# Kernel tuning notes

Hardware: AMD Instinct MI355X
Metric: run time of the kernel (lower is better)

## Reference

```python
import jax, jax.numpy as jnp
import numpy as np

N_PDE = 4096
SENSOR_RANGE = 0.08
WINDOW = int(SENSOR_RANGE * N_PDE)   # 327
HALF = WINDOW // 2                   # 163
RESIZE_LEN = 20
FREQS = jnp.array([1.0, 2.0, 4.0, 8.0], dtype=jnp.float32)
EPS = 1e-6  # flax GroupNorm default epsilon
U_MAX, V_MAX = 40.0, 1.0
N_AGENTS = 262144


def setup_inputs() -> dict:
    key = jax.random.key(0)
    ks = jax.random.split(key, 16)

    def w(k, shape):
        fan_in = shape[0]
        return (jax.random.normal(k, shape, jnp.float32) / np.float32(np.sqrt(fan_in)))

    return {
        "z_curr": jax.random.normal(ks[0], (N_PDE,), jnp.float32),
        "z_target": jax.random.normal(ks[1], (N_PDE,), jnp.float32),
        "xi_curr": jax.random.uniform(ks[2], (N_AGENTS,), jnp.float32),
        # branch net (features=[256,256]), each layer: Dense + GroupNorm(1 group) + tanh
        "bW0": w(ks[3], (2 * RESIZE_LEN, 256)), "bb0": jnp.zeros((256,), jnp.float32),
        "bs0": jnp.ones((256,), jnp.float32), "bB0": jnp.zeros((256,), jnp.float32),
        "bW1": w(ks[4], (256, 256)), "bb1": jnp.zeros((256,), jnp.float32),
        "bs1": jnp.ones((256,), jnp.float32), "bB1": jnp.zeros((256,), jnp.float32),
        # trunk net: 8 -> 32 -> 32
        "tW0": w(ks[5], (8, 32)), "tb0": jnp.zeros((32,), jnp.float32),
        "tW1": w(ks[6], (32, 32)), "tb1": jnp.zeros((32,), jnp.float32),
        # combined head: (256+32) -> 32, then two 32 -> 1 heads
        "cW": w(ks[7], (256 + 32, 32)), "cb": jnp.zeros((32,), jnp.float32),
        "uW": w(ks[8], (32, 1)), "ub": jnp.zeros((1,), jnp.float32),
        "vW": w(ks[9], (32, 1)), "vb": jnp.zeros((1,), jnp.float32),
    }


def _local_obs(padded_error, xi):
    # per-agent dynamic slice + finite-difference gradient + bilinear resize
    center = (xi * (N_PDE - 1)).astype(jnp.int32) + HALF
    start = center - HALF
    p_err = jax.lax.dynamic_slice(padded_error, (start,), (WINDOW,))
    p_grad = jnp.gradient(p_err)
    p_err = jax.image.resize(p_err, (RESIZE_LEN,), method='bilinear')
    p_grad = jax.image.resize(p_grad, (RESIZE_LEN,), method='bilinear')
    return jnp.concatenate([p_err, p_grad])  # [40]


def _groupnorm1(x, scale, bias):
    # GroupNorm(num_groups=1) applied per-sample over the feature axis
    mu = jnp.mean(x, axis=-1, keepdims=True)
    var = jnp.var(x, axis=-1, keepdims=True)
    return (x - mu) * jax.lax.rsqrt(var + EPS) * scale + bias


def reference(z_curr, z_target, xi_curr,
              bW0, bb0, bs0, bB0, bW1, bb1, bs1, bB1,
              tW0, tb0, tW1, tb1, cW, cb, uW, ub, vW, vb):
    error = z_curr - z_target
    padded = jnp.pad(error, (HALF, HALF), mode='edge')  # [N_PDE + 2*HALF]

    patches = jax.vmap(lambda xi: _local_obs(padded, xi))(xi_curr)  # [A, 40]

    # branch net
    h = jnp.tanh(_groupnorm1(patches @ bW0 + bb0, bs0, bB0))  # [A, 256]
    h = jnp.tanh(_groupnorm1(h @ bW1 + bb1, bs1, bB1))        # [A, 256]

    # trunk net
    angle = xi_curr[:, None] * FREQS * jnp.pi                 # [A, 4]
    enc = jnp.concatenate([jnp.sin(angle), jnp.cos(angle)], axis=-1)  # [A, 8]
    enc = jnp.tanh(enc @ tW0 + tb0)
    enc = jnp.tanh(enc @ tW1 + tb1)                           # [A, 32]

    combined = jnp.concatenate([h, enc], axis=-1)             # [A, 288]
    x = jnp.tanh(combined @ cW + cb)                          # [A, 32]
    u_raw = (x @ uW + ub).squeeze(-1)
    v_raw = (x @ vW + vb).squeeze(-1)
    return (U_MAX * jnp.tanh(u_raw), V_MAX * jnp.tanh(v_raw))
```

## Files before the change

kernel.cpp:

```cpp
#include <hip/hip_runtime.h>

#define NP      4096
#define WINDOW  327
#define HALF    163
#define RL      20
#define NA      262144
#define GN_EPS  1e-6f
#define R       8
#define NBLK    (NP / R)
#define NT      512

__device__ __forceinline__ float tanh_fast(float x) {
  float e = __expf(2.0f * x);
  return 1.0f - 2.0f / (e + 1.0f);
}

__device__ __forceinline__ void wave_sum2(float& a, float& b) {
#pragma unroll
  for (int m = 1; m < 64; m <<= 1) {
    a += __shfl_xor(a, m, 64);
    b += __shfl_xor(b, m, 64);
  }
}

#define L_PART  0
#define L_ESP   0
#define L_OBS   336
#define L_HBUF  16384
#define L_HCL   18464
#define L_TOT   18752

__global__ __launch_bounds__(NT, 4) void dc_table(
    const float* __restrict__ zc,  const float* __restrict__ zt,
    const float* __restrict__ bW0, const float* __restrict__ bb0,
    const float* __restrict__ bs0, const float* __restrict__ bB0,
    const float* __restrict__ bW1, const float* __restrict__ bb1,
    const float* __restrict__ bs1, const float* __restrict__ bB1,
    const float* __restrict__ tW0, const float* __restrict__ tb0,
    const float* __restrict__ tW1, const float* __restrict__ tb1,
    const float* __restrict__ cW,  const float* __restrict__ cb,
    const float* __restrict__ uW,  const float* __restrict__ ub,
    const float* __restrict__ vW,  const float* __restrict__ vb,
    float* __restrict__ tbl)
{
  __shared__ __align__(16) float sm[L_TOT];
  float* espan = sm + L_ESP;
  float* obsT  = sm + L_OBS;
  float* part  = sm + L_PART;
  float* hbuf  = sm + L_HBUF;
  float* hcL   = sm + L_HCL;

  const int tid = threadIdx.x;
  const int w   = tid >> 6;
  const int l   = tid & 63;
  const int s0  = blockIdx.x * R;

  if (tid < WINDOW + R - 1) {
    int c = s0 - HALF + tid;
    c = c < 0 ? 0 : (c > NP - 1 ? NP - 1 : c);
    espan[tid] = zc[c] - zt[c];
  }
  __syncthreads();

  {
    const float INV  = (float)WINDOW / (float)RL;
    const float RINV = (float)RL / (float)WINDOW;
    const int sub = tid & 7;
    const int g8  = tid >> 3;
#pragma unroll
    for (int it = 0; it < 5; ++it) {
      int task = it * 64 + g8;
      int q = task % (2 * RL);
      int r = task / (2 * RL);
      int qq = (q < RL) ? q : q - RL;
      float xs = ((float)qq + 0.5f) * INV - 0.5f;
      int jlo = (int)ceilf(xs - INV);  if (jlo < 0) jlo = 0;
      int jhi = (int)floorf(xs + INV); if (jhi > WINDOW - 1) jhi = WINDOW - 1;
      const float* p = espan + r;
      float wsum = 0.0f, vsum = 0.0f;
      for (int j = jlo + sub; j <= jhi; j += 8) {
        float wq = 1.0f - fabsf(xs - (float)j) * RINV;
        float v;
        if (q < RL) {
          v = p[j];
        } else {
          v = (j == 0) ? (p[1] - p[0]) :
              (j == WINDOW - 1) ? (p[WINDOW - 1] - p[WINDOW - 2]) :
              0.5f * (p[j + 1] - p[j - 1]);
        }
        wsum += wq;
        vsum += wq * v;
      }
#pragma unroll
      for (int m = 1; m < 8; m <<= 1) {
        wsum += __shfl_xor(wsum, m, 64);
        vsum += __shfl_xor(vsum, m, 64);
      }
      if (sub == 0) obsT[q * 8 + r] = vsum / wsum;
    }
  }
  __syncthreads();

  float acc[R][4];

#pragma unroll
  for (int r = 0; r < R; ++r) { acc[r][0]=0.f; acc[r][1]=0.f; acc[r][2]=0.f; acc[r][3]=0.f; }
  for (int kk = 0; kk < 5; ++kk) {
    int k = w * 5 + kk;
    float4 wt = *(const float4*)&bW0[k * 256 + 4 * l];
    float4 o0 = *(const float4*)&obsT[k * 8];
    float4 o1 = *(const float4*)&obsT[k * 8 + 4];
    const float wv[4] = {wt.x, wt.y, wt.z, wt.w};
    const float ov[8] = {o0.x, o0.y, o0.z, o0.w, o1.x, o1.y, o1.z, o1.w};
#pragma unroll
    for (int r = 0; r < R; ++r)
#pragma unroll
      for (int j = 0; j < 4; ++j) acc[r][j] = fmaf(ov[r], wv[j], acc[r][j]);
  }
  __syncthreads();

#pragma unroll
  for (int r = 0; r < R; ++r)
    *(float4*)&part[(w << 11) + (r << 8) + 4 * l] = make_float4(acc[r][0], acc[r][1], acc[r][2], acc[r][3]);
  __syncthreads();
  {
    float4 b0 = *(const float4*)&bb0[4 * l];
    float val[4] = {b0.x, b0.y, b0.z, b0.w};
#pragma unroll
    for (int w2 = 0; w2 < 8; ++w2) {
      float4 p0 = *(const float4*)&part[(w2 << 11) + (w << 8) + 4 * l];
      val[0]+=p0.x; val[1]+=p0.y; val[2]+=p0.z; val[3]+=p0.w;
    }
    float s = 0.f, q = 0.f;
#pragma unroll
    for (int i = 0; i < 4; ++i) { s += val[i]; q += val[i] * val[i]; }
    wave_sum2(s, q);
    float mu  = s * (1.0f / 256.0f);
    float var = fmaxf(q * (1.0f / 256.0f) - mu * mu, 0.0f);
    float rv  = rsqrtf(var + GN_EPS);
    float4 sc0 = *(const float4*)&bs0[4 * l];
    float4 sh0 = *(const float4*)&bB0[4 * l];
    const float sc[4] = {sc0.x,sc0.y,sc0.z,sc0.w};
    const float sh[4] = {sh0.x,sh0.y,sh0.z,sh0.w};
    float h[4];
#pragma unroll
    for (int i = 0; i < 4; ++i) h[i] = tanh_fast((val[i] - mu) * rv * sc[i] + sh[i]);
    *(float4*)&hbuf[w * 260 + 4 * l] = make_float4(h[0], h[1], h[2], h[3]);
  }
  __syncthreads();

#pragma unroll
  for (int r = 0; r < R; ++r) { acc[r][0]=0.f; acc[r][1]=0.f; acc[r][2]=0.f; acc[r][3]=0.f; }
  for (int kk = 0; kk < 32; kk += 4) {
    int k0 = w * 32 + kk;
    float4 wt0 = *(const float4*)&bW1[(k0    ) * 256 + 4 * l];
    float4 wt1 = *(const float4*)&bW1[(k0 + 1) * 256 + 4 * l];
    float4 wt2 = *(const float4*)&bW1[(k0 + 2) * 256 + 4 * l];
    float4 wt3 = *(const float4*)&bW1[(k0 + 3) * 256 + 4 * l];
    float4 hr[R];
#pragma unroll
    for (int r = 0; r < R; ++r) hr[r] = *(const float4*)&hbuf[r * 260 + k0];
#pragma unroll
    for (int r = 0; r < R; ++r) {
      const float* hp = (const float*)&hr[r];
      acc[r][0] = fmaf(hp[0], wt0.x, acc[r][0]); acc[r][1] = fmaf(hp[0], wt0.y, acc[r][1]);
      acc[r][2] = fmaf(hp[0], wt0.z, acc[r][2]); acc[r][3] = fmaf(hp[0], wt0.w, acc[r][3]);
      acc[r][0] = fmaf(hp[1], wt1.x, acc[r][0]); acc[r][1] = fmaf(hp[1], wt1.y, acc[r][1]);
      acc[r][2] = fmaf(hp[1], wt1.z, acc[r][2]); acc[r][3] = fmaf(hp[1], wt1.w, acc[r][3]);
      acc[r][0] = fmaf(hp[2], wt2.x, acc[r][0]); acc[r][1] = fmaf(hp[2], wt2.y, acc[r][1]);
      acc[r][2] = fmaf(hp[2], wt2.z, acc[r][2]); acc[r][3] = fmaf(hp[2], wt2.w, acc[r][3]);
      acc[r][0] = fmaf(hp[3], wt3.x, acc[r][0]); acc[r][1] = fmaf(hp[3], wt3.y, acc[r][1]);
      acc[r][2] = fmaf(hp[3], wt3.z, acc[r][2]); acc[r][3] = fmaf(hp[3], wt3.w, acc[r][3]);
    }
  }

#pragma unroll
  for (int r = 0; r < R; ++r)
    *(float4*)&part[(w << 11) + (r << 8) + 4 * l] = make_float4(acc[r][0], acc[r][1], acc[r][2], acc[r][3]);
  __syncthreads();
  {
    float4 b0 = *(const float4*)&bb1[4 * l];
    float val[4] = {b0.x, b0.y, b0.z, b0.w};
#pragma unroll
    for (int w2 = 0; w2 < 8; ++w2) {
      float4 p0 = *(const float4*)&part[(w2 << 11) + (w << 8) + 4 * l];
      val[0]+=p0.x; val[1]+=p0.y; val[2]+=p0.z; val[3]+=p0.w;
    }
    float s = 0.f, q = 0.f;
#pragma unroll
    for (int i = 0; i < 4; ++i) { s += val[i]; q += val[i] * val[i]; }
    wave_sum2(s, q);
    float mu  = s * (1.0f / 256.0f);
    float var = fmaxf(q * (1.0f / 256.0f) - mu * mu, 0.0f);
    float rv  = rsqrtf(var + GN_EPS);
    float4 sc0 = *(const float4*)&bs1[4 * l];
    float4 sh0 = *(const float4*)&bB1[4 * l];
    const float sc[4] = {sc0.x,sc0.y,sc0.z,sc0.w};
    const float sh[4] = {sh0.x,sh0.y,sh0.z,sh0.w};
    float h[4];
#pragma unroll
    for (int i = 0; i < 4; ++i) h[i] = tanh_fast((val[i] - mu) * rv * sc[i] + sh[i]);
    *(float4*)&hbuf[w * 260 + 4 * l] = make_float4(h[0], h[1], h[2], h[3]);
  }
  __syncthreads();

  {
    int r  = w;
    int kg = l >> 3;
    int c  = (l & 7) * 4;
    float ga0 = 0.f, ga1 = 0.f, ga2 = 0.f, ga3 = 0.f;
#pragma unroll
    for (int ii = 0; ii < 8; ++ii) {
      int j  = (ii + kg) & 7;
      int kb = kg * 32 + 4 * j;
      float4 hv = *(const float4*)&hbuf[r * 260 + kb];
      const float hvv[4] = {hv.x, hv.y, hv.z, hv.w};
#pragma unroll
      for (int i2 = 0; i2 < 4; ++i2) {
        float4 cw = *(const float4*)&cW[(kb + i2) * 32 + c];
        ga0 = fmaf(hvv[i2], cw.x, ga0);
        ga1 = fmaf(hvv[i2], cw.y, ga1);
        ga2 = fmaf(hvv[i2], cw.z, ga2);
        ga3 = fmaf(hvv[i2], cw.w, ga3);
      }
    }
#pragma unroll
    for (int m = 8; m < 64; m <<= 1) {
      ga0 += __shfl_xor(ga0, m, 64);
      ga1 += __shfl_xor(ga1, m, 64);
      ga2 += __shfl_xor(ga2, m, 64);
      ga3 += __shfl_xor(ga3, m, 64);
    }
    if (l < 8) {
      float4 cbv = *(const float4*)&cb[c];
      *(float4*)&hcL[r * 36 + c] = make_float4(ga0 + cbv.x, ga1 + cbv.y, ga2 + cbv.z, ga3 + cbv.w);
    }
  }
  __syncthreads();

  if (tid < 128) {
    int v = tid >> 3, sub = tid & 7;
    int r = v >> 1, e = v & 1;
    int jg = s0 + r + e;
    float xe = (float)jg * (1.0f / 4095.0f);
    float enc[8];
#pragma unroll
    for (int k = 0; k < 4; ++k) {
      float fr = (float)(1 << k);
      float a = (xe * fr) * 3.14159265358979f;
      enc[k]     = sinf(a);
      enc[k + 4] = cosf(a);
    }
    int base = (tid & 63) & ~7;

    float t0v[4];
#pragma unroll
    for (int i = 0; i < 4; ++i) {
      int f = 4 * sub + i;
      float a = tb0[f];
#pragma unroll
      for (int k = 0; k < 8; ++k) a = fmaf(enc[k], tW0[k * 32 + f], a);
      t0v[i] = tanh_fast(a);
    }

    float t1v[4];
#pragma unroll
    for (int i = 0; i < 4; ++i) t1v[i] = tb1[4 * sub + i];
#pragma unroll
    for (int j8 = 0; j8 < 8; ++j8) {
#pragma unroll
      for (int i2 = 0; i2 < 4; ++i2) {
        float tv = __shfl(t0v[i2], base + j8, 64);
        int k = 4 * j8 + i2;
#pragma unroll
        for (int i = 0; i < 4; ++i) t1v[i] = fmaf(tv, tW1[k * 32 + 4 * sub + i], t1v[i]);
      }
    }
#pragma unroll
    for (int i = 0; i < 4; ++i) t1v[i] = tanh_fast(t1v[i]);

    float xvv[4];
#pragma unroll
    for (int i = 0; i < 4; ++i) xvv[i] = hcL[r * 36 + 4 * sub + i];
#pragma unroll
    for (int j8 = 0; j8 < 8; ++j8) {
#pragma unroll
      for (int i2 = 0; i2 < 4; ++i2) {
        float tv = __shfl(t1v[i2], base + j8, 64);
        int k = 4 * j8 + i2;
#pragma unroll
        for (int i = 0; i < 4; ++i) xvv[i] = fmaf(tv, cW[(256 + k) * 32 + 4 * sub + i], xvv[i]);
      }
    }
#pragma unroll
    for (int i = 0; i < 4; ++i) xvv[i] = tanh_fast(xvv[i]);

    float up = 0.f, vp = 0.f;
#pragma unroll
    for (int i = 0; i < 4; ++i) {
      up = fmaf(xvv[i], uW[4 * sub + i], up);
      vp = fmaf(xvv[i], vW[4 * sub + i], vp);
    }
#pragma unroll
    for (int m = 1; m < 8; m <<= 1) {
      up += __shfl_xor(up, m, 64);
      vp += __shfl_xor(vp, m, 64);
    }
    if (sub == 0) {
      int s = s0 + r;
      tbl[4 * s + e]     = 40.0f * tanh_fast(up + ub[0]);
      tbl[4 * s + 2 + e] = tanh_fast(vp + vb[0]);
    }
  }
}

__global__ __launch_bounds__(256) void dc_agents(
    const float* __restrict__ xi_curr, const float4* __restrict__ tbl,
    float* __restrict__ out)
{
  int a = blockIdx.x * 256 + threadIdx.x;
  float xi = xi_curr[a];
  float p = xi * 4095.0f;
  int s = (int)p;
  s = s > 4095 ? 4095 : s;
  float t = p - (float)s;
  float4 tb = tbl[s];
  out[a]      = fmaf(t, tb.y - tb.x, tb.x);
  out[NA + a] = fmaf(t, tb.w - tb.z, tb.z);
}

extern "C" void kernel_launch(void* const* d_in, const int* in_sizes, int n_in,
                              void* d_out, int out_size, void* d_ws, size_t ws_size,
                              hipStream_t stream) {
  const float* zc  = (const float*)d_in[0];
  const float* zt  = (const float*)d_in[1];
  const float* xi  = (const float*)d_in[2];
  const float* bW0 = (const float*)d_in[3];
  const float* bb0 = (const float*)d_in[4];
  const float* bs0 = (const float*)d_in[5];
  const float* bB0 = (const float*)d_in[6];
  const float* bW1 = (const float*)d_in[7];
  const float* bb1 = (const float*)d_in[8];
  const float* bs1 = (const float*)d_in[9];
  const float* bB1 = (const float*)d_in[10];
  const float* tW0 = (const float*)d_in[11];
  const float* tb0 = (const float*)d_in[12];
  const float* tW1 = (const float*)d_in[13];
  const float* tb1 = (const float*)d_in[14];
  const float* cW  = (const float*)d_in[15];
  const float* cb  = (const float*)d_in[16];
  const float* uW  = (const float*)d_in[17];
  const float* ub  = (const float*)d_in[18];
  const float* vW  = (const float*)d_in[19];
  const float* vb  = (const float*)d_in[20];

  float* tbl = (float*)d_ws;
  float* out = (float*)d_out;

  dc_table<<<NBLK, NT, 0, stream>>>(zc, zt, bW0, bb0, bs0, bB0,
                                    bW1, bb1, bs1, bB1,
                                    tW0, tb0, tW1, tb1, cW, cb,
                                    uW, ub, vW, vb, tbl);
  dc_agents<<<NA / 256, 256, 0, stream>>>(xi, (const float4*)tbl, out);
}
```

Measured before the change: 122.8 us.

## Halve partial-sum LDS buffer and stage trunk/head weights in shared memory

The cross-wave partial-sum reduction for both branch layers is split into two passes of four rows each, which halves the shared-memory partial buffer and shrinks the block's LDS footprint. The freed space holds copies of the trunk weights, the trunk part of the combined head, and the u/v head weights, so the per-lane scattered global loads in the trunk stage become LDS reads. The split adds an extra barrier pair per layer and leaves half the waves idle during each normalisation pass, in exchange for lower LDS use (possibly more resident blocks) and cheaper weight access.

```diff
diff --git a/kernel.cpp b/kernel.cpp
--- a/kernel.cpp
+++ b/kernel.cpp
@@ -26,9 +26,17 @@
 #define L_PART  0
 #define L_ESP   0
 #define L_OBS   336
-#define L_HBUF  16384
-#define L_HCL   18464
-#define L_TOT   18752
+#define L_HBUF  8192
+#define L_HCL   10272
+#define L_TW1   10560
+#define L_CWT   11584
+#define L_TW0   12608
+#define L_TB0   12864
+#define L_TB1   12896
+#define L_UW    12928
+#define L_VW    12960
+#define L_UVB   12992
+#define L_TOT   12996
 
 __global__ __launch_bounds__(NT, 4) void dc_table(
     const float* __restrict__ zc,  const float* __restrict__ zt,
@@ -49,11 +57,34 @@
   float* part  = sm + L_PART;
   float* hbuf  = sm + L_HBUF;
   float* hcL   = sm + L_HCL;
+  float* tw1s  = sm + L_TW1;
+  float* cwts  = sm + L_CWT;
+  float* tw0s  = sm + L_TW0;
+  float* tb0s  = sm + L_TB0;
+  float* tb1s  = sm + L_TB1;
+  float* uws   = sm + L_UW;
+  float* vws   = sm + L_VW;
+  float* uvb   = sm + L_UVB;
 
   const int tid = threadIdx.x;
   const int w   = tid >> 6;
   const int l   = tid & 63;
   const int s0  = blockIdx.x * R;
+
+  if (tid < 256) {
+    *(float4*)&tw1s[4 * tid] = *(const float4*)&tW1[4 * tid];
+  } else {
+    int t = tid - 256;
+    *(float4*)&cwts[4 * t] = *(const float4*)&cW[256 * 32 + 4 * t];
+  }
+  if (tid < 64) {
+    *(float4*)&tw0s[4 * tid] = *(const float4*)&tW0[4 * tid];
+  } else if (tid < 96)  { tb0s[tid - 64]  = tb0[tid - 64];  }
+  else if (tid < 128)   { tb1s[tid - 96]  = tb1[tid - 96];  }
+  else if (tid < 160)   { uws[tid - 128]  = uW[tid - 128];  }
+  else if (tid < 192)   { vws[tid - 160]  = vW[tid - 160];  }
+  else if (tid == 192)  { uvb[0] = ub[0]; }
+  else if (tid == 193)  { uvb[1] = vb[0]; }
 
   if (tid < WINDOW + R - 1) {
     int c = s0 - HALF + tid;
@@ -120,34 +151,39 @@
   __syncthreads();
 
 #pragma unroll
-  for (int r = 0; r < R; ++r)
-    *(float4*)&part[(w << 11) + (r << 8) + 4 * l] = make_float4(acc[r][0], acc[r][1], acc[r][2], acc[r][3]);
-  __syncthreads();
-  {
-    float4 b0 = *(const float4*)&bb0[4 * l];
-    float val[4] = {b0.x, b0.y, b0.z, b0.w};
-#pragma unroll
-    for (int w2 = 0; w2 < 8; ++w2) {
-      float4 p0 = *(const float4*)&part[(w2 << 11) + (w << 8) + 4 * l];
-      val[0]+=p0.x; val[1]+=p0.y; val[2]+=p0.z; val[3]+=p0.w;
-    }
-    float s = 0.f, q = 0.f;
-#pragma unroll
-    for (int i = 0; i < 4; ++i) { s += val[i]; q += val[i] * val[i]; }
-    wave_sum2(s, q);
-    float mu  = s * (1.0f / 256.0f);
-    float var = fmaxf(q * (1.0f / 256.0f) - mu * mu, 0.0f);
-    float rv  = rsqrtf(var + GN_EPS);
-    float4 sc0 = *(const float4*)&bs0[4 * l];
-    float4 sh0 = *(const float4*)&bB0[4 * l];
-    const float sc[4] = {sc0.x,sc0.y,sc0.z,sc0.w};
-    const float sh[4] = {sh0.x,sh0.y,sh0.z,sh0.w};
-    float h[4];
-#pragma unroll
-    for (int i = 0; i < 4; ++i) h[i] = tanh_fast((val[i] - mu) * rv * sc[i] + sh[i]);
-    *(float4*)&hbuf[w * 260 + 4 * l] = make_float4(h[0], h[1], h[2], h[3]);
-  }
-  __syncthreads();
+  for (int p = 0; p < 2; ++p) {
+#pragma unroll
+    for (int r4 = 0; r4 < 4; ++r4)
+      *(float4*)&part[(w << 10) + (r4 << 8) + 4 * l] =
+        make_float4(acc[4*p+r4][0], acc[4*p+r4][1], acc[4*p+r4][2], acc[4*p+r4][3]);
+    __syncthreads();
+    if (w < 4) {
+      int row = 4 * p + w;
+      float4 b0 = *(const float4*)&bb0[4 * l];
+      float val[4] = {b0.x, b0.y, b0.z, b0.w};
+#pragma unroll
+      for (int w2 = 0; w2 < 8; ++w2) {
+        float4 p0 = *(const float4*)&part[(w2 << 10) + (w << 8) + 4 * l];
+        val[0]+=p0.x; val[1]+=p0.y; val[2]+=p0.z; val[3]+=p0.w;
+      }
+      float s = 0.f, q = 0.f;
+#pragma unroll
+      for (int i = 0; i < 4; ++i) { s += val[i]; q += val[i] * val[i]; }
+      wave_sum2(s, q);
+      float mu  = s * (1.0f / 256.0f);
+      float var = fmaxf(q * (1.0f / 256.0f) - mu * mu, 0.0f);
+      float rv  = rsqrtf(var + GN_EPS);
+      float4 sc0 = *(const float4*)&bs0[4 * l];
+      float4 sh0 = *(const float4*)&bB0[4 * l];
+      const float sc[4] = {sc0.x,sc0.y,sc0.z,sc0.w};
+      const float sh[4] = {sh0.x,sh0.y,sh0.z,sh0.w};
+      float h[4];
+#pragma unroll
+      for (int i = 0; i < 4; ++i) h[i] = tanh_fast((val[i] - mu) * rv * sc[i] + sh[i]);
+      *(float4*)&hbuf[row * 260 + 4 * l] = make_float4(h[0], h[1], h[2], h[3]);
+    }
+    __syncthreads();
+  }
 
 #pragma unroll
   for (int r = 0; r < R; ++r) { acc[r][0]=0.f; acc[r][1]=0.f; acc[r][2]=0.f; acc[r][3]=0.f; }
@@ -175,34 +211,39 @@
   }
 
 #pragma unroll
-  for (int r = 0; r < R; ++r)
-    *(float4*)&part[(w << 11) + (r << 8) + 4 * l] = make_float4(acc[r][0], acc[r][1], acc[r][2], acc[r][3]);
-  __syncthreads();
-  {
-    float4 b0 = *(const float4*)&bb1[4 * l];
-    float val[4] = {b0.x, b0.y, b0.z, b0.w};
-#pragma unroll
-    for (int w2 = 0; w2 < 8; ++w2) {
-      float4 p0 = *(const float4*)&part[(w2 << 11) + (w << 8) + 4 * l];
-      val[0]+=p0.x; val[1]+=p0.y; val[2]+=p0.z; val[3]+=p0.w;
-    }
-    float s = 0.f, q = 0.f;
-#pragma unroll
-    for (int i = 0; i < 4; ++i) { s += val[i]; q += val[i] * val[i]; }
-    wave_sum2(s, q);
-    float mu  = s * (1.0f / 256.0f);
-    float var = fmaxf(q * (1.0f / 256.0f) - mu * mu, 0.0f);
-    float rv  = rsqrtf(var + GN_EPS);
-    float4 sc0 = *(const float4*)&bs1[4 * l];
-    float4 sh0 = *(const float4*)&bB1[4 * l];
-    const float sc[4] = {sc0.x,sc0.y,sc0.z,sc0.w};
-    const float sh[4] = {sh0.x,sh0.y,sh0.z,sh0.w};
-    float h[4];
-#pragma unroll
-    for (int i = 0; i < 4; ++i) h[i] = tanh_fast((val[i] - mu) * rv * sc[i] + sh[i]);
-    *(float4*)&hbuf[w * 260 + 4 * l] = make_float4(h[0], h[1], h[2], h[3]);
-  }
-  __syncthreads();
+  for (int p = 0; p < 2; ++p) {
+#pragma unroll
+    for (int r4 = 0; r4 < 4; ++r4)
+      *(float4*)&part[(w << 10) + (r4 << 8) + 4 * l] =
+        make_float4(acc[4*p+r4][0], acc[4*p+r4][1], acc[4*p+r4][2], acc[4*p+r4][3]);
+    __syncthreads();
+    if (w < 4) {
+      int row = 4 * p + w;
+      float4 b0 = *(const float4*)&bb1[4 * l];
+      float val[4] = {b0.x, b0.y, b0.z, b0.w};
+#pragma unroll
+      for (int w2 = 0; w2 < 8; ++w2) {
+        float4 p0 = *(const float4*)&part[(w2 << 10) + (w << 8) + 4 * l];
+        val[0]+=p0.x; val[1]+=p0.y; val[2]+=p0.z; val[3]+=p0.w;
+      }
+      float s = 0.f, q = 0.f;
+#pragma unroll
+      for (int i = 0; i < 4; ++i) { s += val[i]; q += val[i] * val[i]; }
+      wave_sum2(s, q);
+      float mu  = s * (1.0f / 256.0f);
+      float var = fmaxf(q * (1.0f / 256.0f) - mu * mu, 0.0f);
+      float rv  = rsqrtf(var + GN_EPS);
+      float4 sc0 = *(const float4*)&bs1[4 * l];
+      float4 sh0 = *(const float4*)&bB1[4 * l];
+      const float sc[4] = {sc0.x,sc0.y,sc0.z,sc0.w};
+      const float sh[4] = {sh0.x,sh0.y,sh0.z,sh0.w};
+      float h[4];
+#pragma unroll
+      for (int i = 0; i < 4; ++i) h[i] = tanh_fast((val[i] - mu) * rv * sc[i] + sh[i]);
+      *(float4*)&hbuf[row * 260 + 4 * l] = make_float4(h[0], h[1], h[2], h[3]);
+    }
+    __syncthreads();
+  }
 
   {
     int r  = w;
@@ -257,15 +298,15 @@
 #pragma unroll
     for (int i = 0; i < 4; ++i) {
       int f = 4 * sub + i;
-      float a = tb0[f];
-#pragma unroll
-      for (int k = 0; k < 8; ++k) a = fmaf(enc[k], tW0[k * 32 + f], a);
+      float a = tb0s[f];
+#pragma unroll
+      for (int k = 0; k < 8; ++k) a = fmaf(enc[k], tw0s[k * 32 + f], a);
       t0v[i] = tanh_fast(a);
     }
 
     float t1v[4];
 #pragma unroll
-    for (int i = 0; i < 4; ++i) t1v[i] = tb1[4 * sub + i];
+    for (int i = 0; i < 4; ++i) t1v[i] = tb1s[4 * sub + i];
 #pragma unroll
     for (int j8 = 0; j8 < 8; ++j8) {
 #pragma unroll
@@ -273,7 +314,7 @@
         float tv = __shfl(t0v[i2], base + j8, 64);
         int k = 4 * j8 + i2;
 #pragma unroll
-        for (int i = 0; i < 4; ++i) t1v[i] = fmaf(tv, tW1[k * 32 + 4 * sub + i], t1v[i]);
+        for (int i = 0; i < 4; ++i) t1v[i] = fmaf(tv, tw1s[k * 32 + 4 * sub + i], t1v[i]);
       }
     }
 #pragma unroll
@@ -289,7 +330,7 @@
         float tv = __shfl(t1v[i2], base + j8, 64);
         int k = 4 * j8 + i2;
 #pragma unroll
-        for (int i = 0; i < 4; ++i) xvv[i] = fmaf(tv, cW[(256 + k) * 32 + 4 * sub + i], xvv[i]);
+        for (int i = 0; i < 4; ++i) xvv[i] = fmaf(tv, cwts[k * 32 + 4 * sub + i], xvv[i]);
       }
     }
 #pragma unroll
@@ -298,8 +339,8 @@
     float up = 0.f, vp = 0.f;
 #pragma unroll
     for (int i = 0; i < 4; ++i) {
-      up = fmaf(xvv[i], uW[4 * sub + i], up);
-      vp = fmaf(xvv[i], vW[4 * sub + i], vp);
+      up = fmaf(xvv[i], uws[4 * sub + i], up);
+      vp = fmaf(xvv[i], vws[4 * sub + i], vp);
     }
 #pragma unroll
     for (int m = 1; m < 8; m <<= 1) {
@@ -308,8 +349,8 @@
     }
     if (sub == 0) {
       int s = s0 + r;
-      tbl[4 * s + e]     = 40.0f * tanh_fast(up + ub[0]);
-      tbl[4 * s + 2 + e] = tanh_fast(vp + vb[0]);
+      tbl[4 * s + e]     = 40.0f * tanh_fast(up + uvb[0]);
+      tbl[4 * s + 2 + e] = tanh_fast(vp + uvb[1]);
     }
   }
 }
```

After: 123.0 us. Within noise of the previous version (+0.2%).
